# Optimization experiments

Measured on AMD Instinct MI355X. Metric: run time of the kernel, lower is better.

Reference implementation:

```python
import math
import jax, jax.numpy as jnp
import numpy as np

T_STEPS = 128       # number of diffusion 'experts'
BASE = 64
CH = BASE * 2       # 128 working channels
TE = 256            # time embedding dim
B, IN_C, H, W = 8, 3, 128, 128
EPS = 1e-5


def _conv(x, w, b):
    # x: [N,C,H,W], w: [O,I,3,3] (or 1x1)
    y = jax.lax.conv_general_dilated(x, w, (1, 1), 'SAME',
                                     dimension_numbers=('NCHW', 'OIHW', 'NCHW'))
    return y + b[None, :, None, None]


def _gn(x, scale, bias, groups=8):
    n, c, h, w = x.shape
    xg = x.reshape(n, groups, c // groups, h, w)
    m = xg.mean((2, 3, 4), keepdims=True)
    v = xg.var((2, 3, 4), keepdims=True)
    xn = ((xg - m) * jax.lax.rsqrt(v + EPS)).reshape(n, c, h, w)
    return xn * scale[None, :, None, None] + bias[None, :, None, None]


def setup_inputs() -> dict:
    key = jax.random.key(0)
    ks = iter(jax.random.split(key, 64))
    def p(shape, s=0.05):
        return jax.random.normal(next(ks), shape, jnp.float32) * s
    return {
        'x': jax.random.normal(next(ks), (B, IN_C, H, W), jnp.float32),
        't': jax.random.randint(next(ks), (B,), 0, T_STEPS),
        # feature_extraction
        'fe_w1': p((BASE, IN_C, 3, 3)), 'fe_b1': jnp.zeros((BASE,), jnp.float32),
        'fe_g1s': jnp.ones((BASE,), jnp.float32), 'fe_g1b': jnp.zeros((BASE,), jnp.float32),
        'fe_w2': p((CH, BASE, 3, 3)), 'fe_b2': jnp.zeros((CH,), jnp.float32),
        'fe_g2s': jnp.ones((CH,), jnp.float32), 'fe_g2b': jnp.zeros((CH,), jnp.float32),
        # stacked per-step expert params [T, ...]
        'mlp_w1': p((T_STEPS, TE, TE)), 'mlp_b1': jnp.zeros((T_STEPS, TE), jnp.float32),
        'mlp_w2': p((T_STEPS, CH, TE)), 'mlp_b2': jnp.zeros((T_STEPS, CH), jnp.float32),
        'c1w': p((T_STEPS, CH, CH + 1, 3, 3)), 'c1b': jnp.zeros((T_STEPS, CH), jnp.float32),
        'g1s': jnp.ones((T_STEPS, CH), jnp.float32), 'g1b': jnp.zeros((T_STEPS, CH), jnp.float32),
        'c2w': p((T_STEPS, CH, CH, 3, 3)), 'c2b': jnp.zeros((T_STEPS, CH), jnp.float32),
        'g2s': jnp.ones((T_STEPS, CH), jnp.float32), 'g2b': jnp.zeros((T_STEPS, CH), jnp.float32),
        'c3w': p((T_STEPS, CH, CH, 3, 3)), 'c3b': jnp.zeros((T_STEPS, CH), jnp.float32),
        # color_reconstruction
        'cr_w1': p((BASE, CH, 3, 3)), 'cr_b1': jnp.zeros((BASE,), jnp.float32),
        'cr_gs': jnp.ones((BASE,), jnp.float32), 'cr_gb': jnp.zeros((BASE,), jnp.float32),
        'cr_w2': p((IN_C, BASE, 3, 3)), 'cr_b2': jnp.zeros((IN_C,), jnp.float32),
        # weight_generator (1x1 conv on pooled features)
        'wg_w': p((1, CH, 1, 1)), 'wg_b': jnp.zeros((1,), jnp.float32),
    }


def _expert(xi, tei, w1, b1, w2, b2, cw1, cb1, gs1, gb1, cw2, cb2, gs2, gb2, cw3, cb3):
    # Single-sample DiffusionStep. xi: [C,H,W], tei: [TE]
    h = jax.nn.silu(w1 @ tei + b1)
    tc = (w2 @ h + b2).mean()  # scalar time channel (fix of original view(-1,1,1,1) bug)
    xb = xi[None]  # [1,C,H,W]
    tmap = jnp.broadcast_to(tc, (1, 1) + xi.shape[1:])
    z = jnp.concatenate([xb, tmap], axis=1)  # [1,C+1,H,W]
    z = jax.nn.silu(_gn(_conv(z, cw1, cb1), gs1, gb1))
    z = jax.nn.silu(_gn(_conv(z, cw2, cb2), gs2, gb2))
    z = _conv(z, cw3, cb3)
    return z[0]


def _forward(x, t, fe_w1, fe_b1, fe_g1s, fe_g1b, fe_w2, fe_b2, fe_g2s, fe_g2b,
             mlp_w1, mlp_b1, mlp_w2, mlp_b2, c1w, c1b, g1s, g1b,
             c2w, c2b, g2s, g2b, c3w, c3b,
             cr_w1, cr_b1, cr_gs, cr_gb, cr_w2, cr_b2, wg_w, wg_b):
    feat = jax.nn.silu(_gn(_conv(x, fe_w1, fe_b1), fe_g1s, fe_g1b))
    feat = jax.nn.silu(_gn(_conv(feat, fe_w2, fe_b2), fe_g2s, fe_g2b))  # [B,CH,H,W]

    # sinusoidal time embedding
    half = TE // 2
    freqs = jnp.exp(jnp.arange(half, dtype=jnp.float32) * (-math.log(10000.0) / (half - 1)))
    e = t.astype(jnp.float32)[:, None] * freqs[None, :]
    temb = jnp.concatenate([jnp.sin(e), jnp.cos(e)], axis=-1)  # [B,TE]

    # Each sample matches exactly one step: gather its expert weights, apply once.
    g = lambda a: jnp.take(a, t, axis=0)
    noise = jax.vmap(_expert)(feat, temb,
                              g(mlp_w1), g(mlp_b1), g(mlp_w2), g(mlp_b2),
                              g(c1w), g(c1b), g(g1s), g(g1b),
                              g(c2w), g(c2b), g(g2s), g(g2b),
                              g(c3w), g(c3b))
    alpha = 1.0 - t.astype(jnp.float32) / T_STEPS
    x_t = feat - alpha[:, None, None, None] * noise

    r = jax.nn.silu(_gn(_conv(x_t, cr_w1, cr_b1), cr_gs, cr_gb))
    restored = jax.nn.sigmoid(_conv(r, cr_w2, cr_b2))  # [B,3,H,W]

    pooled = x_t.mean((2, 3))  # adaptive avg pool to 1x1 -> [B,CH]
    weight = jax.nn.sigmoid(pooled @ wg_w[:, :, 0, 0].T + wg_b)[:, :, None, None]  # [B,1,1,1]
    return restored, weight


def reference(x, t, fe_w1, fe_b1, fe_g1s, fe_g1b, fe_w2, fe_b2, fe_g2s, fe_g2b,
              mlp_w1, mlp_b1, mlp_w2, mlp_b2, c1w, c1b, g1s, g1b,
              c2w, c2b, g2s, g2b, c3w, c3b,
              cr_w1, cr_b1, cr_gs, cr_gb, cr_w2, cr_b2, wg_w, wg_b):
    return _forward(x, t, fe_w1, fe_b1, fe_g1s, fe_g1b, fe_w2, fe_b2, fe_g2s, fe_g2b,
                    mlp_w1, mlp_b1, mlp_w2, mlp_b2, c1w, c1b, g1s, g1b,
                    c2w, c2b, g2s, g2b, c3w, c3b,
                    cr_w1, cr_b1, cr_gs, cr_gb, cr_w2, cr_b2, wg_w, wg_b)
```

## Files before the change

kernel.cpp:

```cpp
#include <hip/hip_runtime.h>
#include <hip/hip_bf16.h>

typedef __hip_bfloat16 bf16;

#define HW 128
#define IMG 16384
#define EPSV 1e-5f

typedef __bf16 b16x8 __attribute__((ext_vector_type(8)));
typedef float f32x16 __attribute__((ext_vector_type(16)));

__device__ __forceinline__ float u2f(unsigned int u){ union{unsigned int i; float f;}c; c.i=u; return c.f; }
__device__ __forceinline__ float blo(unsigned int u){ return u2f(u<<16); }
__device__ __forceinline__ float bhi(unsigned int u){ return u2f(u & 0xffff0000u); }
__device__ __forceinline__ unsigned short f2bu(float v){ bf16 h=__float2bfloat16(v); union{bf16 b; unsigned short s;}c; c.b=h; return c.s; }
__device__ __forceinline__ unsigned int pk(float a, float b){ return (unsigned int)f2bu(a) | ((unsigned int)f2bu(b)<<16); }
__device__ __forceinline__ bf16 f2b(float v){ return __float2bfloat16(v); }
__device__ __forceinline__ float sigm(float x){ return 1.f/(1.f+__expf(-x)); }

__device__ __forceinline__ void gload16(const void* g, void* l) {
    __builtin_amdgcn_global_load_lds((const __attribute__((address_space(1))) unsigned int*)(g),
                                     (__attribute__((address_space(3))) unsigned int*)(l), 16, 0, 0);
}

__device__ __forceinline__ f32x16 MFMA(b16x8 a, b16x8 b, f32x16 c){
    return __builtin_amdgcn_mfma_f32_32x32x16_bf16(a, b, c, 0, 0, 0);
}

template<int CIN, int COUT, bool TADD, bool FUSE_GN, bool FUSE_XT>
__global__ void __launch_bounds__(256, 2)
mfma_conv3x3(const bf16* __restrict__ act,
             const bf16* __restrict__ Wt,
             const float* __restrict__ Bt,
             bf16* __restrict__ outp,
             const float* __restrict__ Tt,
             const bf16* __restrict__ zerobuf,
             float* __restrict__ gpart,
             const bf16* __restrict__ featA,
             const int* __restrict__ tsel,
             const float* __restrict__ wgw,
             float* __restrict__ wpart)
{
    static_assert(CIN==64 || CIN==128, "");
    static_assert(COUT==64 || COUT==128, "");
    constexpr int NT  = COUT/64;
    constexpr int CH  = CIN/64;
    constexpr int P   = 9*CH;
    constexpr int WCH = COUT/8;
    constexpr int WSZ = WCH*1024;

    __shared__ char Xb[33792];
    __shared__ char Wa[2][WSZ];
    __shared__ float redS[4][4], redSS[4][4], redW[4];

    const int n    = blockIdx.z;
    const int tile = blockIdx.x;
    const int y0   = tile*2;
    const int tid  = threadIdx.x;
    const int lane = tid & 63;
    const int wid  = tid >> 6;
    const int wm   = wid >> 1;
    const int wn   = wid & 1;
    const int l31  = lane & 31;
    const int lhi  = lane >> 5;

    const bf16* actN = act + (size_t)n * IMG * CIN;
    const bf16* WtN  = Wt  + (size_t)n * 9 * COUT * CIN;

    f32x16 acc[4][NT];
    #pragma unroll
    for (int i=0;i<4;++i)
        #pragma unroll
        for (int j=0;j<NT;++j)
            #pragma unroll
            for (int k=0;k<16;++k) acc[i][j][k] = 0.f;

    auto stage_X = [&](int dy, int ch) {
        const int ry0 = y0 + dy - 1;
        for (int u = wid; u < 33; u += 4) {
            int s = u*8 + (lane>>3);
            int g = lane & 7;
            int r  = (s >= 130) ? 1 : 0;
            int xp = s - r*130;
            int xx = xp - 1;
            int ry = ry0 + r;
            const void* src = zerobuf;
            if (s < 260 && (unsigned)xx < 128u && (unsigned)ry < 128u)
                src = actN + ((size_t)(ry*128 + xx)*CIN + ch*64 + 8*(g ^ (s&7)));
            gload16(src, Xb + u*1024);
        }
    };
    auto stage_W = [&](int r, int ch, int buf) {
        for (int u = wid; u < WCH; u += 4) {
            int co = u*8 + (lane>>3);
            int g  = lane & 7;
            const void* src = WtN + ((size_t)(r*COUT + co)*CIN + ch*64 + 8*(g ^ (co&7)));
            gload16(src, Wa[buf] + u*1024);
        }
    };

    stage_X(0, 0);
    stage_W(0, 0, 0);
    __syncthreads();

    int buf = 0;
    for (int p = 0; p < P; ++p) {
        const int dx = p % 3;
        const int pc = p / 3;
        const int ch = pc % CH;
        const int dy = pc / CH;
        const bool last = (p+1 == P);

        if (!last) {
            const int pn  = p + 1;
            const int ndx = pn % 3;
            const int npc = pn / 3;
            const int nch = npc % CH;
            const int ndy = npc / CH;
            stage_W(ndy*3 + ndx, nch, buf ^ 1);
        }
        (void)dy; (void)ch;

        __builtin_amdgcn_s_setprio(1);
        #pragma unroll
        for (int s = 0; s < 4; ++s) {
            const int koff = s*32 + lhi*16;
            b16x8 bfr[NT];
            #pragma unroll
            for (int q = 0; q < NT; ++q) {
                int co = wn*32*NT + q*32 + l31;
                bfr[q] = *(const b16x8*)(Wa[buf] + co*128 + (koff ^ ((co&7)<<4)));
            }
            b16x8 afr[4];
            #pragma unroll
            for (int mt = 0; mt < 4; ++mt) {
                int sl = wm*130 + mt*32 + l31 + dx;
                afr[mt] = *(const b16x8*)(Xb + sl*128 + (koff ^ ((sl&7)<<4)));
            }
            #pragma unroll
            for (int mt = 0; mt < 4; ++mt)
                #pragma unroll
                for (int q = 0; q < NT; ++q)
                    acc[mt][q] = MFMA(afr[mt], bfr[q], acc[mt][q]);
        }
        __builtin_amdgcn_s_setprio(0);

        if (!last) {
            if (dx == 2) {
                __syncthreads();
                const int pn  = p + 1;
                const int npc = pn / 3;
                stage_X(npc / CH, npc % CH);
                __syncthreads();
            } else {
                __syncthreads();
            }
        }
        buf ^= 1;
    }

    const float* BtN = Bt + n*COUT;
    const int y = y0 + wm;
    bf16* outRow = outp + ((size_t)n*IMG + (size_t)y*128)*COUT;
    const bf16* featRow = FUSE_XT ? (featA + ((size_t)n*IMG + (size_t)y*128)*COUT) : nullptr;
    float alpha = 0.f;
    if (FUSE_XT) alpha = 1.f - (float)tsel[n] * (1.f/128.f);

    float gs[NT], gss[NT], wsum = 0.f;
    #pragma unroll
    for (int q = 0; q < NT; ++q) { gs[q]=0.f; gss[q]=0.f; }

    #pragma unroll
    for (int q = 0; q < NT; ++q) {
        const int co = wn*32*NT + q*32 + l31;
        const float bv = BtN[co];
        float wg = 0.f;
        if (FUSE_XT) wg = wgw[co];
        float T0=0.f, T1=0.f, T2=0.f;
        if (TADD) {
            int yt = (y==0) ? 0 : (y==127 ? 2 : 1);
            const float* Tp = Tt + (size_t)(n*COUT + co)*9 + yt*3;
            T0 = Tp[0]; T1 = Tp[1]; T2 = Tp[2];
        }
        #pragma unroll
        for (int mt = 0; mt < 4; ++mt) {
            #pragma unroll
            for (int reg = 0; reg < 16; ++reg) {
                const int x = mt*32 + (reg&3) + 8*(reg>>2) + 4*lhi;
                float v = acc[mt][q][reg] + bv;
                if (TADD) v += (x==0) ? T0 : (x==127 ? T2 : T1);
                if (FUSE_GN) { gs[q] += v; gss[q] += v*v; }
                if (FUSE_XT) {
                    float fv = __bfloat162float(featRow[(size_t)x*COUT + co]);
                    float xt = fv - alpha*v;
                    outRow[(size_t)x*COUT + co] = f2b(xt);
                    wsum += xt * wg;
                } else {
                    outRow[(size_t)x*COUT + co] = f2b(v);
                }
            }
        }
    }

    if (FUSE_GN) {
        constexpr int LG = (COUT==128) ? 4 : 3;
        #pragma unroll
        for (int q = 0; q < NT; ++q) {
            float a = gs[q], b = gss[q];
            #pragma unroll
            for (int m = 1; m < (1<<LG); m <<= 1) { a += __shfl_xor(a, m); b += __shfl_xor(b, m); }
            a += __shfl_xor(a, 32); b += __shfl_xor(b, 32);
            const int co = wn*32*NT + q*32 + l31;
            if (lhi == 0 && (l31 & ((1<<LG)-1)) == 0) {
                int j = (co >> LG) & 3;
                redS[wid][j] = a; redSS[wid][j] = b;
            }
        }
        __syncthreads();
        if (tid < 8) {
            int g = tid, wn_ = g>>2, j = g&3;
            float S  = redS[wn_][j]  + redS[2+wn_][j];
            float SS = redSS[wn_][j] + redSS[2+wn_][j];
            gpart[((size_t)(n*64 + tile))*16 + 2*g]     = S;
            gpart[((size_t)(n*64 + tile))*16 + 2*g + 1] = SS;
        }
    }
    if (FUSE_XT) {
        float a = wsum;
        #pragma unroll
        for (int m = 1; m < 64; m <<= 1) a += __shfl_xor(a, m);
        if (lane == 0) redW[wid] = a;
        __syncthreads();
        if (tid == 0) wpart[n*64 + tile] = redW[0]+redW[1]+redW[2]+redW[3];
    }
}

__global__ void __launch_bounds__(256)
wtprep_kernel(const float* __restrict__ w, const float* __restrict__ b,
              const int* __restrict__ t, bf16* __restrict__ Wt, float* __restrict__ Bt,
              int CO, int COsrc, int CIN, int CINW, int gather)
{
    int idx = blockIdx.x*256 + threadIdx.x;
    int total = 8*9*CO*CIN;
    if (idx >= total) return;
    int cin = idx & (CIN-1);
    int tmp = idx / CIN;
    int co  = tmp % CO;
    int tmp2 = tmp / CO;
    int r   = tmp2 % 9;
    int n   = tmp2 / 9;
    int sel = gather ? t[n] : 0;
    float v = 0.f;
    if (co < COsrc) v = w[(((size_t)sel*COsrc + co)*CINW + cin)*9 + r];
    Wt[idx] = f2b(v);
    if (cin==0 && r==0) Bt[n*CO+co] = (co < COsrc) ? b[(size_t)sel*COsrc + co] : 0.f;
}

__global__ void __launch_bounds__(256)
tprep_kernel(const int* __restrict__ t, const float* __restrict__ c1w,
             const float* __restrict__ tc, float* __restrict__ Tt)
{
    int idx = blockIdx.x*256 + threadIdx.x;
    if (idx >= 8*128) return;
    int n = idx >> 7, co = idx & 127;
    const float* wp = c1w + ((size_t)t[n]*128 + co)*129*9 + 128*9;
    float w9[9];
    #pragma unroll
    for (int i=0;i<9;++i) w9[i] = wp[i];
    float tcv = tc[n];
    #pragma unroll
    for (int yt=0; yt<3; ++yt)
        #pragma unroll
        for (int xt=0; xt<3; ++xt) {
            float s = 0.f;
            #pragma unroll
            for (int dy=0; dy<3; ++dy)
                #pragma unroll
                for (int dx=0; dx<3; ++dx) {
                    bool vy = (yt==0) ? (dy>=1) : ((yt==2) ? (dy<=1) : true);
                    bool vx = (xt==0) ? (dx>=1) : ((xt==2) ? (dx<=1) : true);
                    if (vy && vx) s += w9[dy*3+dx];
                }
            Tt[(size_t)idx*9 + yt*3+xt] = tcv*s;
        }
}

__global__ void __launch_bounds__(256)
fe1_kernel(const float* __restrict__ in, const float* __restrict__ w,
           const float* __restrict__ bias, bf16* __restrict__ out)
{
    const int n   = blockIdx.z;
    const int co0 = blockIdx.y * 8;
    const int tx0 = (blockIdx.x & 7) * 16;
    const int ty0 = (blockIdx.x >> 3) * 16;
    const int lx = threadIdx.x & 15, ly = threadIdx.x >> 4;
    __shared__ float tileS[18][19];
    float acc[8];
    #pragma unroll
    for (int i=0;i<8;++i) acc[i] = bias[co0+i];
    const float* inN = in + (size_t)n*3*IMG;
    for (int ci=0; ci<3; ++ci) {
        __syncthreads();
        for (int idx = threadIdx.x; idx < 18*18; idx += 256) {
            int tyy = idx/18, txx = idx - tyy*18;
            int gy = ty0+tyy-1, gx = tx0+txx-1;
            float v = 0.f;
            if ((unsigned)gy < 128u && (unsigned)gx < 128u) v = inN[ci*IMG + gy*128+gx];
            tileS[tyy][txx] = v;
        }
        __syncthreads();
        float v[9];
        #pragma unroll
        for (int ky=0;ky<3;++ky)
            #pragma unroll
            for (int kx=0;kx<3;++kx) v[ky*3+kx] = tileS[ly+ky][lx+kx];
        #pragma unroll
        for (int c=0;c<8;++c) {
            const float* wp = w + ((co0+c)*3 + ci)*9;
            #pragma unroll
            for (int k=0;k<9;++k) acc[c] = fmaf(v[k], wp[k], acc[c]);
        }
    }
    int gy = ty0+ly, gx = tx0+lx;
    uint4 o; o.x = pk(acc[0],acc[1]); o.y = pk(acc[2],acc[3]);
    o.z = pk(acc[4],acc[5]); o.w = pk(acc[6],acc[7]);
    *(uint4*)(out + ((size_t)n*IMG + gy*128+gx)*64 + co0) = o;
}

template<int C>
__global__ void __launch_bounds__(256)
gn_stats_nhwc(const bf16* __restrict__ x, float* __restrict__ partials)
{
    constexpr int L2CPG = (C==128) ? 4 : 3;
    const int chunk = blockIdx.x, n = blockIdx.y;
    const int t = threadIdx.x;
    const uint4* pv = (const uint4*)(x + ((size_t)n*IMG + chunk*256 + t)*C);
    float s[8], ss[8];
    #pragma unroll
    for (int g=0; g<8; ++g) { s[g]=0.f; ss[g]=0.f; }
    #pragma unroll
    for (int v=0; v<C/8; ++v) {
        int g = (v*8) >> L2CPG;
        uint4 u = pv[v];
        float f0=blo(u.x), f1=bhi(u.x), f2=blo(u.y), f3=bhi(u.y);
        float f4=blo(u.z), f5=bhi(u.z), f6=blo(u.w), f7=bhi(u.w);
        s[g]  += ((f0+f1)+(f2+f3)) + ((f4+f5)+(f6+f7));
        ss[g] += ((f0*f0+f1*f1)+(f2*f2+f3*f3)) + ((f4*f4+f5*f5)+(f6*f6+f7*f7));
    }
    __shared__ float sh[16][256];
    #pragma unroll
    for (int g=0; g<8; ++g) { sh[2*g][t] = s[g]; sh[2*g+1][t] = ss[g]; }
    __syncthreads();
    for (int off=128; off>0; off>>=1) {
        if (t < off) {
            #pragma unroll
            for (int k=0;k<16;++k) sh[k][t] += sh[k][t+off];
        }
        __syncthreads();
    }
    if (t < 16) partials[((size_t)n*64 + chunk)*16 + t] = sh[t][0];
}

__global__ void __launch_bounds__(128)
gn_final(const float* __restrict__ partials, const float* __restrict__ scale,
         const float* __restrict__ bias, const int* __restrict__ tsel,
         int C, int l2cpg, float* __restrict__ scA, float* __restrict__ biA)
{
    int n = blockIdx.x, c = threadIdx.x;
    if (c >= C) return;
    int g = c >> l2cpg;
    float s=0.f, ss=0.f;
    for (int k=0;k<64;++k) {
        s  += partials[((size_t)n*64+k)*16 + 2*g];
        ss += partials[((size_t)n*64+k)*16 + 2*g + 1];
    }
    float cnt = (float)IMG * (float)(C>>3);
    float m = s/cnt, var = ss/cnt - m*m;
    float r = rsqrtf(var + EPSV);
    int po = tsel ? tsel[n]*C : 0;
    float sc = scale[po+c]*r;
    scA[n*C+c] = sc;
    biA[n*C+c] = bias[po+c] - m*sc;
}

template<int C>
__global__ void __launch_bounds__(256)
gn_apply_nhwc(bf16* __restrict__ x, const float* __restrict__ scA, const float* __restrict__ biA)
{
    size_t e0 = ((size_t)blockIdx.x*256 + threadIdx.x)*8;
    int n = (int)(e0 >> ((C==128) ? 21 : 20));
    int c0 = (int)(e0 & (C-1));
    const float4 sA = *(const float4*)(scA + n*C + c0);
    const float4 sB = *(const float4*)(scA + n*C + c0 + 4);
    const float4 bA = *(const float4*)(biA + n*C + c0);
    const float4 bB = *(const float4*)(biA + n*C + c0 + 4);
    uint4* p = (uint4*)(x + e0);
    uint4 u = *p;
    float f[8] = {blo(u.x),bhi(u.x),blo(u.y),bhi(u.y),blo(u.z),bhi(u.z),blo(u.w),bhi(u.w)};
    f[0]=f[0]*sA.x+bA.x; f[1]=f[1]*sA.y+bA.y; f[2]=f[2]*sA.z+bA.z; f[3]=f[3]*sA.w+bA.w;
    f[4]=f[4]*sB.x+bB.x; f[5]=f[5]*sB.y+bB.y; f[6]=f[6]*sB.z+bB.z; f[7]=f[7]*sB.w+bB.w;
    #pragma unroll
    for (int i=0;i<8;++i) f[i] = f[i]*sigm(f[i]);
    u.x = pk(f[0],f[1]); u.y = pk(f[2],f[3]); u.z = pk(f[4],f[5]); u.w = pk(f[6],f[7]);
    *p = u;
}

__global__ void __launch_bounds__(256)
time_mlp_kernel(const int* __restrict__ t,
                const float* __restrict__ w1, const float* __restrict__ b1,
                const float* __restrict__ w2, const float* __restrict__ b2,
                float* __restrict__ tc)
{
    const int n = blockIdx.x;
    const int ti = t[n];
    const int tid = threadIdx.x;
    __shared__ float temb[256];
    __shared__ float h[256];
    {
        int j = tid & 127;
        float fr = expf(-9.210340371976184f / 127.f * (float)j);
        float e = (float)ti * fr;
        temb[tid] = (tid < 128) ? sinf(e) : cosf(e);
    }
    __syncthreads();
    {
        const float* w1p = w1 + ((size_t)ti * 256 + tid) * 256;
        float s = b1[(size_t)ti * 256 + tid];
        for (int j = 0; j < 256; ++j) s += w1p[j] * temb[j];
        h[tid] = s * sigm(s);
    }
    __syncthreads();
    float part = 0.f;
    if (tid < 128) {
        const float* w2p = w2 + ((size_t)ti * 128 + tid) * 256;
        float s = b2[(size_t)ti * 128 + tid];
        for (int j = 0; j < 256; ++j) s += w2p[j] * h[j];
        part = s;
    }
    __shared__ float red[256];
    red[tid] = part;
    __syncthreads();
    for (int off = 128; off > 0; off >>= 1) {
        if (tid < off) red[tid] += red[tid + off];
        __syncthreads();
    }
    if (tid == 0) tc[n] = red[0] * (1.f / 128.f);
}

__global__ void __launch_bounds__(64)
weight_final_kernel(const float* __restrict__ wpart, const float* __restrict__ wg_b,
                    float* __restrict__ outw)
{
    const int n = blockIdx.x;
    float s = wpart[n*64 + threadIdx.x];
    #pragma unroll
    for (int m = 1; m < 64; m <<= 1) s += __shfl_xor(s, m);
    if (threadIdx.x == 0) outw[n] = sigm(s * (1.f/16384.f) + wg_b[0]);
}

__global__ void __launch_bounds__(256)
extract_kernel(const bf16* __restrict__ in, float* __restrict__ out)
{
    int n = blockIdx.y;
    int px = blockIdx.x*256 + threadIdx.x;
    const bf16* p = in + ((size_t)n*IMG + px)*64;
    float r0 = __bfloat162float(p[0]);
    float r1 = __bfloat162float(p[1]);
    float r2 = __bfloat162float(p[2]);
    size_t ob = (size_t)n*3*IMG + px;
    out[ob]         = sigm(r0);
    out[ob + IMG]   = sigm(r1);
    out[ob + 2*IMG] = sigm(r2);
}

extern "C" void kernel_launch(void* const* d_in, const int* in_sizes, int n_in,
                              void* d_out, int out_size, void* d_ws, size_t ws_size,
                              hipStream_t stream)
{
    (void)in_sizes; (void)n_in; (void)out_size; (void)ws_size;

    const float* x      = (const float*)d_in[0];
    const int*   t      = (const int*)  d_in[1];
    const float* fe_w1  = (const float*)d_in[2];
    const float* fe_b1  = (const float*)d_in[3];
    const float* fe_g1s = (const float*)d_in[4];
    const float* fe_g1b = (const float*)d_in[5];
    const float* fe_w2  = (const float*)d_in[6];
    const float* fe_b2  = (const float*)d_in[7];
    const float* fe_g2s = (const float*)d_in[8];
    const float* fe_g2b = (const float*)d_in[9];
    const float* mlp_w1 = (const float*)d_in[10];
    const float* mlp_b1 = (const float*)d_in[11];
    const float* mlp_w2 = (const float*)d_in[12];
    const float* mlp_b2 = (const float*)d_in[13];
    const float* c1w    = (const float*)d_in[14];
    const float* c1b    = (const float*)d_in[15];
    const float* g1s    = (const float*)d_in[16];
    const float* g1b    = (const float*)d_in[17];
    const float* c2w    = (const float*)d_in[18];
    const float* c2b    = (const float*)d_in[19];
    const float* g2s    = (const float*)d_in[20];
    const float* g2b    = (const float*)d_in[21];
    const float* c3w    = (const float*)d_in[22];
    const float* c3b    = (const float*)d_in[23];
    const float* cr_w1  = (const float*)d_in[24];
    const float* cr_b1  = (const float*)d_in[25];
    const float* cr_gs  = (const float*)d_in[26];
    const float* cr_gb  = (const float*)d_in[27];
    const float* cr_w2  = (const float*)d_in[28];
    const float* cr_b2  = (const float*)d_in[29];
    const float* wg_w   = (const float*)d_in[30];
    const float* wg_b   = (const float*)d_in[31];

    char* ws = (char*)d_ws;
    bf16* A   = (bf16*)(ws);
    bf16* Bb  = (bf16*)(ws + 33554432);
    bf16* Cb  = (bf16*)(ws + 67108864);
    bf16* Wt  = (bf16*)(ws + 100663296);
    float* Bt = (float*)(ws + 103022592);
    float* Tt = (float*)(ws + 103026688);
    float* tc = (float*)(ws + 103063552);
    bf16* zb  = (bf16*)(ws + 103063616);
    float* gp = (float*)(ws + 103063680);
    float* scA = (float*)(ws + 103096448);
    float* biA = (float*)(ws + 103100544);
    float* wp  = (float*)(ws + 103104640);

    float* out_img = (float*)d_out;
    float* out_w   = out_img + 393216;

    dim3 blk(256);
    dim3 cgrid(64, 1, 8);
    hipMemsetAsync(zb, 0, 64, stream);

    time_mlp_kernel<<<8, blk, 0, stream>>>(t, mlp_w1, mlp_b1, mlp_w2, mlp_b2, tc);
    tprep_kernel<<<4, blk, 0, stream>>>(t, c1w, tc, Tt);

    fe1_kernel<<<dim3(64, 8, 8), blk, 0, stream>>>(x, fe_w1, fe_b1, Bb);
    gn_stats_nhwc<64><<<dim3(64, 8), blk, 0, stream>>>(Bb, gp);
    gn_final<<<8, 128, 0, stream>>>(gp, fe_g1s, fe_g1b, nullptr, 64, 3, scA, biA);
    gn_apply_nhwc<64><<<4096, blk, 0, stream>>>(Bb, scA, biA);

    wtprep_kernel<<<2304, blk, 0, stream>>>(fe_w2, fe_b2, t, Wt, Bt, 128, 128, 64, 64, 0);
    mfma_conv3x3<64,128,false,true,false><<<cgrid, blk, 0, stream>>>(Bb, Wt, Bt, A, nullptr, zb, gp, nullptr, nullptr, nullptr, nullptr);
    gn_final<<<8, 128, 0, stream>>>(gp, fe_g2s, fe_g2b, nullptr, 128, 4, scA, biA);
    gn_apply_nhwc<128><<<8192, blk, 0, stream>>>(A, scA, biA);

    wtprep_kernel<<<4608, blk, 0, stream>>>(c1w, c1b, t, Wt, Bt, 128, 128, 128, 129, 1);
    mfma_conv3x3<128,128,true,true,false><<<cgrid, blk, 0, stream>>>(A, Wt, Bt, Bb, Tt, zb, gp, nullptr, nullptr, nullptr, nullptr);
    gn_final<<<8, 128, 0, stream>>>(gp, g1s, g1b, t, 128, 4, scA, biA);
    gn_apply_nhwc<128><<<8192, blk, 0, stream>>>(Bb, scA, biA);

    wtprep_kernel<<<4608, blk, 0, stream>>>(c2w, c2b, t, Wt, Bt, 128, 128, 128, 128, 1);
    mfma_conv3x3<128,128,false,true,false><<<cgrid, blk, 0, stream>>>(Bb, Wt, Bt, Cb, nullptr, zb, gp, nullptr, nullptr, nullptr, nullptr);
    gn_final<<<8, 128, 0, stream>>>(gp, g2s, g2b, t, 128, 4, scA, biA);
    gn_apply_nhwc<128><<<8192, blk, 0, stream>>>(Cb, scA, biA);

    wtprep_kernel<<<4608, blk, 0, stream>>>(c3w, c3b, t, Wt, Bt, 128, 128, 128, 128, 1);
    mfma_conv3x3<128,128,false,false,true><<<cgrid, blk, 0, stream>>>(Cb, Wt, Bt, Bb, nullptr, zb, nullptr, A, t, wg_w, wp);
    weight_final_kernel<<<8, 64, 0, stream>>>(wp, wg_b, out_w);

    wtprep_kernel<<<2304, blk, 0, stream>>>(cr_w1, cr_b1, t, Wt, Bt, 64, 64, 128, 128, 0);
    mfma_conv3x3<128,64,false,true,false><<<cgrid, blk, 0, stream>>>(Bb, Wt, Bt, Cb, nullptr, zb, gp, nullptr, nullptr, nullptr, nullptr);
    gn_final<<<8, 128, 0, stream>>>(gp, cr_gs, cr_gb, nullptr, 64, 3, scA, biA);
    gn_apply_nhwc<64><<<4096, blk, 0, stream>>>(Cb, scA, biA);

    wtprep_kernel<<<1152, blk, 0, stream>>>(cr_w2, cr_b2, t, Wt, Bt, 64, 3, 64, 64, 0);
    mfma_conv3x3<64,64,false,false,false><<<cgrid, blk, 0, stream>>>(Cb, Wt, Bt, A, nullptr, zb, nullptr, nullptr, nullptr, nullptr, nullptr);
    extract_kernel<<<dim3(64, 8), blk, 0, stream>>>(A, out_img);
}
```

Measured before the change: 375.7 us.

## Split conv tile across 8 waves instead of 4 to raise occupancy

The MFMA 3x3 conv kernel now launches 512 threads per block, 8 waves, with each wave owning half the pixel columns of a row and half the output channels. Per-wave accumulators shrink from 4xNT to 2xNQ tiles, which lowers register pressure so more waves can hide LDS and global latency. In exchange, each B fragment is reused across fewer A fragments, so more LDS reads are issued per MFMA, and the group-norm and weight reductions are reworked for 8 waves.

Result: no change. 369.4 us (-1.7%).

```diff
diff --git a/kernel.cpp b/kernel.cpp
--- a/kernel.cpp
+++ b/kernel.cpp
@@ -28,7 +28,7 @@
 }
 
 template<int CIN, int COUT, bool TADD, bool FUSE_GN, bool FUSE_XT>
-__global__ void __launch_bounds__(256, 2)
+__global__ void __launch_bounds__(512, 4)
 mfma_conv3x3(const bf16* __restrict__ act,
              const bf16* __restrict__ Wt,
              const float* __restrict__ Bt,
@@ -43,7 +43,7 @@
 {
     static_assert(CIN==64 || CIN==128, "");
     static_assert(COUT==64 || COUT==128, "");
-    constexpr int NT  = COUT/64;
+    constexpr int NQ  = COUT/64;
     constexpr int CH  = CIN/64;
     constexpr int P   = 9*CH;
     constexpr int WCH = COUT/8;
@@ -51,7 +51,7 @@
 
     __shared__ char Xb[33792];
     __shared__ char Wa[2][WSZ];
-    __shared__ float redS[4][4], redSS[4][4], redW[4];
+    __shared__ float redS[8][4], redSS[8][4], redW[8];
 
     const int n    = blockIdx.z;
     const int tile = blockIdx.x;
@@ -59,27 +59,28 @@
     const int tid  = threadIdx.x;
     const int lane = tid & 63;
     const int wid  = tid >> 6;
-    const int wm   = wid >> 1;
-    const int wn   = wid & 1;
+    const int row  = wid >> 2;
+    const int coh  = (wid >> 1) & 1;
+    const int pxh  = wid & 1;
     const int l31  = lane & 31;
     const int lhi  = lane >> 5;
+    const int g    = lane & 7;
 
     const bf16* actN = act + (size_t)n * IMG * CIN;
     const bf16* WtN  = Wt  + (size_t)n * 9 * COUT * CIN;
 
-    f32x16 acc[4][NT];
-    #pragma unroll
-    for (int i=0;i<4;++i)
-        #pragma unroll
-        for (int j=0;j<NT;++j)
+    f32x16 acc[2][NQ];
+    #pragma unroll
+    for (int i=0;i<2;++i)
+        #pragma unroll
+        for (int j=0;j<NQ;++j)
             #pragma unroll
             for (int k=0;k<16;++k) acc[i][j][k] = 0.f;
 
     auto stage_X = [&](int dy, int ch) {
         const int ry0 = y0 + dy - 1;
-        for (int u = wid; u < 33; u += 4) {
+        for (int u = wid; u < 33; u += 8) {
             int s = u*8 + (lane>>3);
-            int g = lane & 7;
             int r  = (s >= 130) ? 1 : 0;
             int xp = s - r*130;
             int xx = xp - 1;
@@ -91,9 +92,8 @@
         }
     };
     auto stage_W = [&](int r, int ch, int buf) {
-        for (int u = wid; u < WCH; u += 4) {
+        for (int u = wid; u < WCH; u += 8) {
             int co = u*8 + (lane>>3);
-            int g  = lane & 7;
             const void* src = WtN + ((size_t)(r*COUT + co)*CIN + ch*64 + 8*(g ^ (co&7)));
             gload16(src, Wa[buf] + u*1024);
         }
@@ -106,41 +106,35 @@
     int buf = 0;
     for (int p = 0; p < P; ++p) {
         const int dx = p % 3;
-        const int pc = p / 3;
-        const int ch = pc % CH;
-        const int dy = pc / CH;
         const bool last = (p+1 == P);
 
         if (!last) {
             const int pn  = p + 1;
             const int ndx = pn % 3;
             const int npc = pn / 3;
-            const int nch = npc % CH;
-            const int ndy = npc / CH;
-            stage_W(ndy*3 + ndx, nch, buf ^ 1);
-        }
-        (void)dy; (void)ch;
+            stage_W((npc/CH)*3 + ndx, npc % CH, buf ^ 1);
+        }
 
         __builtin_amdgcn_s_setprio(1);
         #pragma unroll
-        for (int s = 0; s < 4; ++s) {
-            const int koff = s*32 + lhi*16;
-            b16x8 bfr[NT];
-            #pragma unroll
-            for (int q = 0; q < NT; ++q) {
-                int co = wn*32*NT + q*32 + l31;
+        for (int s4 = 0; s4 < 4; ++s4) {
+            const int koff = s4*32 + lhi*16;
+            b16x8 bfr[NQ];
+            #pragma unroll
+            for (int q = 0; q < NQ; ++q) {
+                int co = coh*32*NQ + q*32 + l31;
                 bfr[q] = *(const b16x8*)(Wa[buf] + co*128 + (koff ^ ((co&7)<<4)));
             }
-            b16x8 afr[4];
-            #pragma unroll
-            for (int mt = 0; mt < 4; ++mt) {
-                int sl = wm*130 + mt*32 + l31 + dx;
+            b16x8 afr[2];
+            #pragma unroll
+            for (int mt = 0; mt < 2; ++mt) {
+                int sl = row*130 + (pxh*2+mt)*32 + l31 + dx;
                 afr[mt] = *(const b16x8*)(Xb + sl*128 + (koff ^ ((sl&7)<<4)));
             }
             #pragma unroll
-            for (int mt = 0; mt < 4; ++mt)
+            for (int mt = 0; mt < 2; ++mt)
                 #pragma unroll
-                for (int q = 0; q < NT; ++q)
+                for (int q = 0; q < NQ; ++q)
                     acc[mt][q] = MFMA(afr[mt], bfr[q], acc[mt][q]);
         }
         __builtin_amdgcn_s_setprio(0);
@@ -148,8 +142,7 @@
         if (!last) {
             if (dx == 2) {
                 __syncthreads();
-                const int pn  = p + 1;
-                const int npc = pn / 3;
+                const int npc = (p + 1) / 3;
                 stage_X(npc / CH, npc % CH);
                 __syncthreads();
             } else {
@@ -160,19 +153,19 @@
     }
 
     const float* BtN = Bt + n*COUT;
-    const int y = y0 + wm;
+    const int y = y0 + row;
     bf16* outRow = outp + ((size_t)n*IMG + (size_t)y*128)*COUT;
     const bf16* featRow = FUSE_XT ? (featA + ((size_t)n*IMG + (size_t)y*128)*COUT) : nullptr;
     float alpha = 0.f;
     if (FUSE_XT) alpha = 1.f - (float)tsel[n] * (1.f/128.f);
 
-    float gs[NT], gss[NT], wsum = 0.f;
-    #pragma unroll
-    for (int q = 0; q < NT; ++q) { gs[q]=0.f; gss[q]=0.f; }
-
-    #pragma unroll
-    for (int q = 0; q < NT; ++q) {
-        const int co = wn*32*NT + q*32 + l31;
+    float gs[NQ], gss[NQ], wsum = 0.f;
+    #pragma unroll
+    for (int q = 0; q < NQ; ++q) { gs[q]=0.f; gss[q]=0.f; }
+
+    #pragma unroll
+    for (int q = 0; q < NQ; ++q) {
+        const int co = coh*32*NQ + q*32 + l31;
         const float bv = BtN[co];
         float wg = 0.f;
         if (FUSE_XT) wg = wgw[co];
@@ -183,10 +176,10 @@
             T0 = Tp[0]; T1 = Tp[1]; T2 = Tp[2];
         }
         #pragma unroll
-        for (int mt = 0; mt < 4; ++mt) {
+        for (int mt = 0; mt < 2; ++mt) {
             #pragma unroll
             for (int reg = 0; reg < 16; ++reg) {
-                const int x = mt*32 + (reg&3) + 8*(reg>>2) + 4*lhi;
+                const int x = pxh*64 + mt*32 + (reg&3) + 8*(reg>>2) + 4*lhi;
                 float v = acc[mt][q][reg] + bv;
                 if (TADD) v += (x==0) ? T0 : (x==127 ? T2 : T1);
                 if (FUSE_GN) { gs[q] += v; gss[q] += v*v; }
@@ -205,24 +198,26 @@
     if (FUSE_GN) {
         constexpr int LG = (COUT==128) ? 4 : 3;
         #pragma unroll
-        for (int q = 0; q < NT; ++q) {
+        for (int q = 0; q < NQ; ++q) {
             float a = gs[q], b = gss[q];
             #pragma unroll
             for (int m = 1; m < (1<<LG); m <<= 1) { a += __shfl_xor(a, m); b += __shfl_xor(b, m); }
             a += __shfl_xor(a, 32); b += __shfl_xor(b, 32);
-            const int co = wn*32*NT + q*32 + l31;
             if (lhi == 0 && (l31 & ((1<<LG)-1)) == 0) {
-                int j = (co >> LG) & 3;
-                redS[wid][j] = a; redSS[wid][j] = b;
+                int jp = (COUT==128) ? (q*2 + (l31>>4)) : (l31>>3);
+                redS[wid][jp] = a; redSS[wid][jp] = b;
             }
         }
         __syncthreads();
         if (tid < 8) {
-            int g = tid, wn_ = g>>2, j = g&3;
-            float S  = redS[wn_][j]  + redS[2+wn_][j];
-            float SS = redSS[wn_][j] + redSS[2+wn_][j];
-            gpart[((size_t)(n*64 + tile))*16 + 2*g]     = S;
-            gpart[((size_t)(n*64 + tile))*16 + 2*g + 1] = SS;
+            int gg = tid;
+            float S = 0.f, SS = 0.f;
+            #pragma unroll
+            for (int w = 0; w < 8; ++w) {
+                if (((w>>1)&1) == (gg>>2)) { S += redS[w][gg&3]; SS += redSS[w][gg&3]; }
+            }
+            gpart[((size_t)(n*64 + tile))*16 + 2*gg]     = S;
+            gpart[((size_t)(n*64 + tile))*16 + 2*gg + 1] = SS;
         }
     }
     if (FUSE_XT) {
@@ -231,7 +226,12 @@
         for (int m = 1; m < 64; m <<= 1) a += __shfl_xor(a, m);
         if (lane == 0) redW[wid] = a;
         __syncthreads();
-        if (tid == 0) wpart[n*64 + tile] = redW[0]+redW[1]+redW[2]+redW[3];
+        if (tid == 0) {
+            float s = 0.f;
+            #pragma unroll
+            for (int w = 0; w < 8; ++w) s += redW[w];
+            wpart[n*64 + tile] = s;
+        }
     }
 }
 
@@ -530,6 +530,7 @@
     float* out_w   = out_img + 393216;
 
     dim3 blk(256);
+    dim3 cblk(512);
     dim3 cgrid(64, 1, 8);
     hipMemsetAsync(zb, 0, 64, stream);
 
@@ -542,30 +543,36 @@
     gn_apply_nhwc<64><<<4096, blk, 0, stream>>>(Bb, scA, biA);
 
     wtprep_kernel<<<2304, blk, 0, stream>>>(fe_w2, fe_b2, t, Wt, Bt, 128, 128, 64, 64, 0);
-    mfma_conv3x3<64,128,false,true,false><<<cgrid, blk, 0, stream>>>(Bb, Wt, Bt, A, nullptr, zb, gp, nullptr, nullptr, nullptr, nullptr);
+    mfma_conv3x3<64,128,false,true,false><<<cgrid, cblk, 0, stream>>>(
+        Bb, Wt, Bt, A, nullptr, zb, gp, nullptr, nullptr, nullptr, nullptr);
     gn_final<<<8, 128, 0, stream>>>(gp, fe_g2s, fe_g2b, nullptr, 128, 4, scA, biA);
     gn_apply_nhwc<128><<<8192, blk, 0, stream>>>(A, scA, biA);
 
     wtprep_kernel<<<4608, blk, 0, stream>>>(c1w, c1b, t, Wt, Bt, 128, 128, 128, 129, 1);
-    mfma_conv3x3<128,128,true,true,false><<<cgrid, blk, 0, stream>>>(A, Wt, Bt, Bb, Tt, zb, gp, nullptr, nullptr, nullptr, nullptr);
+    mfma_conv3x3<128,128,true,true,false><<<cgrid, cblk, 0, stream>>>(
+        A, Wt, Bt, Bb, Tt, zb, gp, nullptr, nullptr, nullptr, nullptr);
     gn_final<<<8, 128, 0, stream>>>(gp, g1s, g1b, t, 128, 4, scA, biA);
     gn_apply_nhwc<128><<<8192, blk, 0, stream>>>(Bb, scA, biA);
 
     wtprep_kernel<<<4608, blk, 0, stream>>>(c2w, c2b, t, Wt, Bt, 128, 128, 128, 128, 1);
-    mfma_conv3x3<128,128,false,true,false><<<cgrid, blk, 0, stream>>>(Bb, Wt, Bt, Cb, nullptr, zb, gp, nullptr, nullptr, nullptr, nullptr);
+    mfma_conv3x3<128,128,false,true,false><<<cgrid, cblk, 0, stream>>>(
+        Bb, Wt, Bt, Cb, nullptr, zb, gp, nullptr, nullptr, nullptr, nullptr);
     gn_final<<<8, 128, 0, stream>>>(gp, g2s, g2b, t, 128, 4, scA, biA);
     gn_apply_nhwc<128><<<8192, blk, 0, stream>>>(Cb, scA, biA);
 
     wtprep_kernel<<<4608, blk, 0, stream>>>(c3w, c3b, t, Wt, Bt, 128, 128, 128, 128, 1);
-    mfma_conv3x3<128,128,false,false,true><<<cgrid, blk, 0, stream>>>(Cb, Wt, Bt, Bb, nullptr, zb, nullptr, A, t, wg_w, wp);
+    mfma_conv3x3<128,128,false,false,true><<<cgrid, cblk, 0, stream>>>(
+        Cb, Wt, Bt, Bb, nullptr, zb, nullptr, A, t, wg_w, wp);
     weight_final_kernel<<<8, 64, 0, stream>>>(wp, wg_b, out_w);
 
     wtprep_kernel<<<2304, blk, 0, stream>>>(cr_w1, cr_b1, t, Wt, Bt, 64, 64, 128, 128, 0);
-    mfma_conv3x3<128,64,false,true,false><<<cgrid, blk, 0, stream>>>(Bb, Wt, Bt, Cb, nullptr, zb, gp, nullptr, nullptr, nullptr, nullptr);
+    mfma_conv3x3<128,64,false,true,false><<<cgrid, cblk, 0, stream>>>(
+        Bb, Wt, Bt, Cb, nullptr, zb, gp, nullptr, nullptr, nullptr, nullptr);
     gn_final<<<8, 128, 0, stream>>>(gp, cr_gs, cr_gb, nullptr, 64, 3, scA, biA);
     gn_apply_nhwc<64><<<4096, blk, 0, stream>>>(Cb, scA, biA);
 
     wtprep_kernel<<<1152, blk, 0, stream>>>(cr_w2, cr_b2, t, Wt, Bt, 64, 3, 64, 64, 0);
-    mfma_conv3x3<64,64,false,false,false><<<cgrid, blk, 0, stream>>>(Cb, Wt, Bt, A, nullptr, zb, nullptr, nullptr, nullptr, nullptr, nullptr);
+    mfma_conv3x3<64,64,false,false,false><<<cgrid, cblk, 0, stream>>>(
+        Cb, Wt, Bt, A, nullptr, zb, nullptr, nullptr, nullptr, nullptr, nullptr);
     extract_kernel<<<dim3(64, 8), blk, 0, stream>>>(A, out_img);
 }
```
